# Performance work log

Measured on AMD Instinct MI355X. Metric: run time of the kernel, lower is better.

The kernel has to match this reference:

```python
import jax, jax.numpy as jnp
import numpy as np

N = 100000   # nodes / embedding vocab
E = 1600000  # edges
D = 128      # feature dim
R = 7        # num relations
B = 4096     # matches
EPS = 1e-5


def setup_inputs() -> dict:
    key = jax.random.key(0)
    ks = jax.random.split(key, 12)
    s = 0.05
    return {
        "x": jnp.arange(N, dtype=jnp.int32),
        "edge_index": jax.random.randint(ks[0], (2, E), 0, N, dtype=jnp.int32),
        "edge_type": jax.random.randint(ks[1], (E,), 0, R, dtype=jnp.int32),
        "home": jax.random.randint(ks[2], (B,), 0, N, dtype=jnp.int32),
        "away": jax.random.randint(ks[3], (B,), 0, N, dtype=jnp.int32),
        "embed": jax.random.normal(ks[4], (N, D), jnp.float32) * s,
        "rel_w": jax.random.normal(ks[5], (3, R, D, D), jnp.float32) * s,
        "root_w": jax.random.normal(ks[6], (3, D, D), jnp.float32) * s,
        "conv_b": jnp.zeros((3, D), jnp.float32),
        "bn_gamma": jnp.ones((2, D), jnp.float32),
        "bn_beta": jnp.zeros((2, D), jnp.float32),
        "bn_mean": jnp.zeros((2, D), jnp.float32),
        "bn_var": jnp.ones((2, D), jnp.float32),
        "fc0_w": jax.random.normal(ks[7], (256, 2 * D), jnp.float32) * s,
        "fc0_b": jnp.zeros((256,), jnp.float32),
        "fc1_w": jax.random.normal(ks[8], (128, 256), jnp.float32) * s,
        "fc1_b": jnp.zeros((128,), jnp.float32),
        "fc2_w": jax.random.normal(ks[9], (3, 128), jnp.float32) * s,
        "fc2_b": jnp.zeros((3,), jnp.float32),
    }


def rgcn_conv(h, rel_w, root_w, bias, src, dst, seg):
    # PyG RGCNConv with aggr='mean': per-relation mean of source features,
    # aggregate-then-transform (valid since the relation transform is linear).
    n = h.shape[0]
    agg = jax.ops.segment_sum(h[src], seg, num_segments=n * R)      # [N*R, Din]
    cnt = jax.ops.segment_sum(jnp.ones((src.shape[0],), h.dtype), seg,
                              num_segments=n * R)                   # [N*R]
    agg = (agg / jnp.maximum(cnt, 1.0)[:, None]).reshape(n, R, -1)  # [N, R, Din]
    return jnp.einsum('nri,rio->no', agg, rel_w) + h @ root_w + bias


def reference(x, edge_index, edge_type, home, away, embed, rel_w, root_w, conv_b,
              bn_gamma, bn_beta, bn_mean, bn_var,
              fc0_w, fc0_b, fc1_w, fc1_b, fc2_w, fc2_b):
    src, dst = edge_index[0], edge_index[1]
    seg = dst.astype(jnp.int32) * R + edge_type  # combined (node, relation) id

    h = embed[x]  # [N, D]
    for l in range(2):
        h = rgcn_conv(h, rel_w[l], root_w[l], conv_b[l], src, dst, seg)
        h = (h - bn_mean[l]) * jax.lax.rsqrt(bn_var[l] + EPS) * bn_gamma[l] + bn_beta[l]
        h = jax.nn.relu(h)
    h = rgcn_conv(h, rel_w[2], root_w[2], conv_b[2], src, dst, seg)

    g = jnp.concatenate([h[home], h[away]], axis=1)  # [B, 2D]
    g = jax.nn.relu(g @ fc0_w.T + fc0_b)
    g = jax.nn.relu(g @ fc1_w.T + fc1_b)
    g = g @ fc2_w.T + fc2_b
    return jax.nn.log_softmax(g, axis=1)
```

## Files before the change

kernel.cpp:

```cpp
#include <hip/hip_runtime.h>
#include <hip/hip_bf16.h>

#define RR 7
#define EPSBN 1e-5f

typedef __attribute__((ext_vector_type(8))) __bf16 bf16x8;
typedef __attribute__((ext_vector_type(4))) float f32x4;
typedef __attribute__((ext_vector_type(2))) float f32x2;

__device__ __forceinline__ float uhi2f(unsigned int u) {
    union { unsigned int i; float f; } c; c.i = u; return c.f;
}
__device__ __forceinline__ unsigned short f2b(float f) {
    union { float f; unsigned int i; } c; c.f = f;
    unsigned int x = c.i;
    return (unsigned short)((x + 0x7fffu + ((x >> 16) & 1u)) >> 16);
}

__global__ void hist_k(const int* __restrict__ dst, const int* __restrict__ et,
                       int* __restrict__ cnt, int* __restrict__ rank, int ne) {
    int e = blockIdx.x * 256 + threadIdx.x;
    if (e < ne) rank[e] = atomicAdd(&cnt[dst[e] * RR + et[e]], 1);
}
__global__ void scan1_k(const int* __restrict__ cnt, int* __restrict__ bsum, int n) {
    __shared__ int sh[256];
    int base = blockIdx.x << 10;
    int s = 0;
    for (int i = threadIdx.x; i < 1024; i += 256) { int idx = base + i; if (idx < n) s += cnt[idx]; }
    sh[threadIdx.x] = s; __syncthreads();
    for (int off = 128; off > 0; off >>= 1) {
        if (threadIdx.x < off) sh[threadIdx.x] += sh[threadIdx.x + off];
        __syncthreads();
    }
    if (threadIdx.x == 0) bsum[blockIdx.x] = sh[0];
}
__global__ void scan2_k(int* __restrict__ bsum, int nb) {
    __shared__ int sh[256];
    int t = threadIdx.x;
    int v[4]; int loc = 0;
#pragma unroll
    for (int i = 0; i < 4; ++i) { int idx = t * 4 + i; v[i] = (idx < nb) ? bsum[idx] : 0; loc += v[i]; }
    sh[t] = loc; __syncthreads();
    for (int off = 1; off < 256; off <<= 1) {
        int x = (t >= off) ? sh[t - off] : 0;
        __syncthreads();
        sh[t] += x;
        __syncthreads();
    }
    int ex = (t > 0) ? sh[t - 1] : 0;
#pragma unroll
    for (int i = 0; i < 4; ++i) { int idx = t * 4 + i; if (idx < nb) { int vv = v[i]; bsum[idx] = ex; ex += vv; } }
}
__global__ void scan3_k(const int* __restrict__ cnt, const int* __restrict__ boff,
                        int* __restrict__ ptr, int n, int total) {
    __shared__ int sh[256];
    int t = threadIdx.x;
    int base = (blockIdx.x << 10) + (t << 2);
    int v[4]; int loc = 0;
#pragma unroll
    for (int i = 0; i < 4; ++i) { int idx = base + i; v[i] = (idx < n) ? cnt[idx] : 0; loc += v[i]; }
    sh[t] = loc; __syncthreads();
    for (int off = 1; off < 256; off <<= 1) {
        int x = (t >= off) ? sh[t - off] : 0;
        __syncthreads();
        sh[t] += x;
        __syncthreads();
    }
    int ex = boff[blockIdx.x] + ((t > 0) ? sh[t - 1] : 0);
#pragma unroll
    for (int i = 0; i < 4; ++i) {
        int idx = base + i;
        if (idx < n) { ptr[idx] = ex; ex += v[i]; }
    }
    if (blockIdx.x == 0 && t == 0) ptr[n] = total;
}
__global__ void scatter_k(const int* __restrict__ src, const int* __restrict__ dst,
                          const int* __restrict__ et, const int* __restrict__ rank,
                          const int* __restrict__ ptr, int* __restrict__ ssorted, int ne) {
    int e = blockIdx.x * 256 + threadIdx.x;
    if (e < ne) {
        int seg = dst[e] * RR + et[e];
        ssorted[ptr[seg] + rank[e]] = src[e];
    }
    if (blockIdx.x == 0 && threadIdx.x < 16) ssorted[ne + threadIdx.x] = 0;
}

__global__ void mark_k(const int* __restrict__ home, const int* __restrict__ away,
                       const int* __restrict__ ptr, const int* __restrict__ ssorted,
                       int* __restrict__ mark, int* __restrict__ list,
                       int* __restrict__ count, int Bn) {
    int i = blockIdx.x * 256 + threadIdx.x;
    if (i >= 2 * Bn) return;
    int node = (i < Bn) ? home[i] : away[i - Bn];
    if (atomicExch(&mark[node], 1) == 0) { int p = atomicAdd(count, 1); list[p] = node; }
    int e0 = ptr[node * RR], e1 = ptr[node * RR + RR];
    for (int e = e0; e < e1; ++e) {
        int s = ssorted[e];
        if (atomicExch(&mark[s], 1) == 0) { int p = atomicAdd(count, 1); list[p] = s; }
    }
}

__global__ __launch_bounds__(256) void prep_all_k(
    const float* __restrict__ rel_w, const float* __restrict__ root_w,
    unsigned short* __restrict__ wall,
    const int* __restrict__ x, const float* __restrict__ embed,
    unsigned short* __restrict__ h, int n, int nhb,
    const float* __restrict__ fc0w, const float* __restrict__ fc1w,
    float* __restrict__ w0t, float* __restrict__ w1t,
    const float* __restrict__ conv_b,
    const float* __restrict__ bn_g, const float* __restrict__ bn_b,
    const float* __restrict__ bn_m, const float* __restrict__ bn_v,
    float* __restrict__ AB)
{
    __shared__ unsigned short T[128][130];
    int b = blockIdx.x;
    int t = threadIdx.x;
    if (b < 24) {
        int l = b >> 3, kb = b & 7;
        const float* src = (kb < RR) ? rel_w + ((size_t)(l * RR + kb) << 14)
                                     : root_w + ((size_t)l << 14);
        for (int c = t; c < 4096; c += 256) {
            float4 f = *(const float4*)(src + (c << 2));
            int i = c >> 5, o = (c & 31) << 2;
            T[i][o] = f2b(f.x); T[i][o+1] = f2b(f.y); T[i][o+2] = f2b(f.z); T[i][o+3] = f2b(f.w);
        }
        __syncthreads();
        unsigned short* dst = wall + ((size_t)b << 14);
        for (int c = t; c < 2048; c += 256) {
            int frag = c >> 6;
            int lane = c & 63;
            int ks = frag >> 3, nt = frag & 7;
            int o = (nt << 4) + (lane & 15);
            int ib = (ks << 5) + ((lane >> 4) << 3);
            uint4 o4;
            o4.x = (unsigned)T[ib+0][o] | ((unsigned)T[ib+1][o] << 16);
            o4.y = (unsigned)T[ib+2][o] | ((unsigned)T[ib+3][o] << 16);
            o4.z = (unsigned)T[ib+4][o] | ((unsigned)T[ib+5][o] << 16);
            o4.w = (unsigned)T[ib+6][o] | ((unsigned)T[ib+7][o] << 16);
            *(uint4*)(dst + (c << 3)) = o4;
        }
    } else if (b < 24 + nhb) {
        int i = (b - 24) * 256 + t;
        if (i < n * 16) {
            int node = i >> 4, c8 = (i & 15) << 3;
            const float* e = embed + ((size_t)x[node] << 7) + c8;
            float4 f0 = *(const float4*)e;
            float4 f1 = *(const float4*)(e + 4);
            uint4 o4;
            o4.x = (unsigned)f2b(f0.x) | ((unsigned)f2b(f0.y) << 16);
            o4.y = (unsigned)f2b(f0.z) | ((unsigned)f2b(f0.w) << 16);
            o4.z = (unsigned)f2b(f1.x) | ((unsigned)f2b(f1.y) << 16);
            o4.w = (unsigned)f2b(f1.z) | ((unsigned)f2b(f1.w) << 16);
            *(uint4*)(h + ((size_t)node << 7) + c8) = o4;
        }
    } else if (b < 24 + nhb + 256) {
        int idx = ((b - 24 - nhb) << 8) + t;
        int o = idx & 255, i = idx >> 8;
        w0t[idx] = fc0w[o * 256 + i];
    } else if (b < 24 + nhb + 384) {
        int idx = ((b - 24 - nhb - 256) << 8) + t;
        int o = idx & 127, i = idx >> 7;
        w1t[idx] = fc1w[o * 256 + i];
    } else {
        for (int q = t; q < 384; q += 256) {
            int l = q >> 7, j = q & 127;
            float A = 1.f, Bv = conv_b[(l << 7) + j];
            if (l < 2) {
                float sc = bn_g[(l << 7) + j] * rsqrtf(bn_v[(l << 7) + j] + EPSBN);
                A = sc;
                Bv = Bv * sc + (bn_b[(l << 7) + j] - bn_m[(l << 7) + j] * sc);
            }
            AB[(l << 8) + j] = A;
            AB[(l << 8) + 128 + j] = Bv;
        }
    }
}

#define PAIRF(pw) ((f32x2){uhi2f((pw) << 16), uhi2f((pw) & 0xffff0000u)})
#define ACCP(b, u) { av2[(b)+0] += PAIRF((u).x); av2[(b)+1] += PAIRF((u).y); \
                     av2[(b)+2] += PAIRF((u).z); av2[(b)+3] += PAIRF((u).w); }
#define GATH(s) { const unsigned short* hp = h_in + ((size_t)(s) << 7) + (quad << 3); \
                  uint4 u0 = *(const uint4*)(hp);       uint4 u1 = *(const uint4*)(hp + 32); \
                  uint4 u2 = *(const uint4*)(hp + 64);  uint4 u3 = *(const uint4*)(hp + 96); \
                  ACCP(0, u0); ACCP(4, u1); ACCP(8, u2); ACCP(12, u3); }

__global__ __launch_bounds__(128, 4) void layer_k(
    const unsigned short* __restrict__ h_in,
    unsigned short* __restrict__ h_out,
    const unsigned short* __restrict__ wfrag,
    const float* __restrict__ AB,
    const int* __restrict__ seg_ptr, const int* __restrict__ src_sorted,
    const int* __restrict__ list_a, const int* __restrict__ list_b, int listB,
    const int* __restrict__ nout_dev,
    int nout, int bnrelu, int by_node)
{
    const int tid  = threadIdx.x;
    const int wave = tid >> 6;
    const int lane = tid & 63;
    const int n16  = lane & 15;
    const int quad = lane >> 4;
    const int row0 = blockIdx.x << 5;
    if (nout_dev) nout = *nout_dev;
    if (row0 >= nout) return;
    const int gidx = row0 + (wave << 4) + n16;
    const bool valid = gidx < nout;
    int gnode = 0;
    if (valid) {
        gnode = list_a ? (gidx < listB ? list_a[gidx] : list_b[gidx - listB]) : gidx;
    }

    int p[8];
    {
        int b = valid ? gnode * RR : 0;
#pragma unroll
        for (int i = 0; i < 8; ++i) p[i] = seg_ptr[b + i];
    }

    f32x4 acc[8];
#pragma unroll
    for (int i = 0; i < 8; ++i) acc[i] = (f32x4){0.f, 0.f, 0.f, 0.f};

    int sv0, sv1, sv2, sv3;
    { int e0 = p[0]; sv0 = src_sorted[e0]; sv1 = src_sorted[e0+1];
      sv2 = src_sorted[e0+2]; sv3 = src_sorted[e0+3]; }

    const unsigned short* wl = wfrag + (lane << 3);

#pragma unroll
    for (int kb = 0; kb < 8; ++kb) {
        f32x2 av2[16];
#pragma unroll
        for (int i = 0; i < 16; ++i) av2[i] = (f32x2){0.f, 0.f};
        float scale = 1.f;
        int nv0 = 0, nv1 = 0, nv2 = 0, nv3 = 0;
        if (kb < RR) {
            if (kb < RR - 1) {
                int en = p[kb + 1];
                nv0 = src_sorted[en]; nv1 = src_sorted[en+1];
                nv2 = src_sorted[en+2]; nv3 = src_sorted[en+3];
            }
            if (valid) {
                int e0 = p[kb], e1 = p[kb + 1];
                int cnt = e1 - e0;
                if (cnt > 0) scale = __builtin_amdgcn_rcpf((float)cnt);
                if (cnt > 0) GATH(sv0);
                if (cnt > 1) GATH(sv1);
                if (cnt > 2) GATH(sv2);
                if (cnt > 3) GATH(sv3);
                for (int e = e0 + 4; e < e1; ++e) {
                    int s = src_sorted[e];
                    GATH(s);
                }
            }
        } else {
            if (valid) GATH(gnode);
        }
        uint4 au[4];
#pragma unroll
        for (int ks = 0; ks < 4; ++ks) {
            unsigned pw[4];
#pragma unroll
            for (int m = 0; m < 4; ++m) {
                f32x2 q = av2[(ks << 2) + m] * scale;
                __hip_bfloat162 b2 = __float22bfloat162_rn(make_float2(q.x, q.y));
                unsigned uu; __builtin_memcpy(&uu, &b2, 4);
                pw[m] = uu;
            }
            au[ks].x = pw[0]; au[ks].y = pw[1]; au[ks].z = pw[2]; au[ks].w = pw[3];
        }
        const unsigned short* wk = wl + (kb << 14);
#pragma unroll
        for (int ks = 0; ks < 4; ++ks) {
            bf16x8 af;
            __builtin_memcpy(&af, &au[ks], 16);
#pragma unroll
            for (int nt = 0; nt < 8; ++nt) {
                bf16x8 bfr = *(const bf16x8*)(wk + (((ks << 3) + nt) << 9));
                acc[nt] = __builtin_amdgcn_mfma_f32_16x16x32_bf16(af, bfr, acc[nt], 0, 0, 0);
            }
        }
        sv0 = nv0; sv1 = nv1; sv2 = nv2; sv3 = nv3;
    }

    int orow[4];
#pragma unroll
    for (int r = 0; r < 4; ++r) {
        int ri = row0 + (wave << 4) + (quad << 2) + r;
        if (ri < nout) {
            orow[r] = by_node ? (ri < listB ? list_a[ri] : list_b[ri - listB]) : ri;
        } else orow[r] = -1;
    }
#pragma unroll
    for (int nt = 0; nt < 8; ++nt) {
        int j = (nt << 4) + n16;
        float Aj = AB[j];
        float Bj = AB[128 + j];
#pragma unroll
        for (int r = 0; r < 4; ++r) {
            if (orow[r] >= 0) {
                float v = acc[nt][r] * Aj + Bj;
                if (bnrelu) v = fmaxf(v, 0.f);
                h_out[((size_t)orow[r] << 7) + j] = f2b(v);
            }
        }
    }
}

__global__ __launch_bounds__(256) void mlp_k(
    const unsigned short* __restrict__ hC,
    const float* __restrict__ w0t, const float* __restrict__ bb0,
    const float* __restrict__ w1t, const float* __restrict__ bb1,
    const float* __restrict__ w2, const float* __restrict__ bb2,
    float* __restrict__ out, int Bn)
{
    __shared__ __attribute__((aligned(16))) float g0[16][256];
    __shared__ __attribute__((aligned(16))) float g1[16][256];
    __shared__ float lg[16][4];
    int t = threadIdx.x;
    {
        int row = t >> 4;
        int cseg = (t & 15) << 4;
        int gr = (blockIdx.x << 4) + row;
        int gc = (gr < Bn) ? gr : 0;
        const unsigned short* sp = (cseg < 128) ? (hC + ((size_t)gc << 7) + cseg)
                                                : (hC + ((size_t)(Bn + gc) << 7) + (cseg - 128));
#pragma unroll
        for (int c8 = 0; c8 < 2; ++c8) {
            uint4 v = *(const uint4*)(sp + (c8 << 3));
            int base = cseg + (c8 << 3);
            g0[row][base+0] = uhi2f(v.x << 16); g0[row][base+1] = uhi2f(v.x & 0xffff0000u);
            g0[row][base+2] = uhi2f(v.y << 16); g0[row][base+3] = uhi2f(v.y & 0xffff0000u);
            g0[row][base+4] = uhi2f(v.z << 16); g0[row][base+5] = uhi2f(v.z & 0xffff0000u);
            g0[row][base+6] = uhi2f(v.w << 16); g0[row][base+7] = uhi2f(v.w & 0xffff0000u);
        }
    }
    __syncthreads();
    {
        float acc[16];
#pragma unroll
        for (int r = 0; r < 16; ++r) acc[r] = 0.f;
#pragma unroll 4
        for (int i = 0; i < 256; ++i) {
            float w = w0t[(i << 8) + t];
#pragma unroll
            for (int r = 0; r < 16; ++r) acc[r] += w * g0[r][i];
        }
        float bb = bb0[t];
#pragma unroll
        for (int r = 0; r < 16; ++r) g1[r][t] = fmaxf(acc[r] + bb, 0.f);
    }
    __syncthreads();
    {
        int o = t & 127, rg = t >> 7;
        float acc[8];
#pragma unroll
        for (int r = 0; r < 8; ++r) acc[r] = 0.f;
#pragma unroll 4
        for (int i = 0; i < 256; ++i) {
            float w = w1t[(i << 7) + o];
#pragma unroll
            for (int r = 0; r < 8; ++r) acc[r] += w * g1[(rg << 3) + r][i];
        }
        float bb = bb1[o];
#pragma unroll
        for (int r = 0; r < 8; ++r) g0[(rg << 3) + r][o] = fmaxf(acc[r] + bb, 0.f);
    }
    __syncthreads();
    if (t < 48) {
        int row = t / 3, cls = t - row * 3;
        const float* wr = w2 + (cls << 7);
        float a = 0.f;
        for (int i = 0; i < 128; i += 4) {
            float4 w = *(const float4*)(wr + i);
            float4 g = *(const float4*)&g0[row][i];
            a += w.x * g.x + w.y * g.y + w.z * g.z + w.w * g.w;
        }
        lg[row][cls] = a + bb2[cls];
    }
    __syncthreads();
    if (t < 16) {
        int gr = (blockIdx.x << 4) + t;
        if (gr < Bn) {
            float l0 = lg[t][0], l1 = lg[t][1], l2 = lg[t][2];
            float m = fmaxf(l0, fmaxf(l1, l2));
            float lse = m + logf(expf(l0 - m) + expf(l1 - m) + expf(l2 - m));
            out[gr * 3 + 0] = l0 - lse;
            out[gr * 3 + 1] = l1 - lse;
            out[gr * 3 + 2] = l2 - lse;
        }
    }
}

extern "C" void kernel_launch(void* const* d_in, const int* in_sizes, int n_in,
                              void* d_out, int out_size, void* d_ws, size_t ws_size,
                              hipStream_t stream) {
    const int*   x      = (const int*)d_in[0];
    const int*   eidx   = (const int*)d_in[1];
    const int*   etype  = (const int*)d_in[2];
    const int*   home   = (const int*)d_in[3];
    const int*   away   = (const int*)d_in[4];
    const float* embed  = (const float*)d_in[5];
    const float* rel_w  = (const float*)d_in[6];
    const float* root_w = (const float*)d_in[7];
    const float* conv_b = (const float*)d_in[8];
    const float* bn_g   = (const float*)d_in[9];
    const float* bn_b   = (const float*)d_in[10];
    const float* bn_m   = (const float*)d_in[11];
    const float* bn_v   = (const float*)d_in[12];
    const float* fc0w   = (const float*)d_in[13];
    const float* fc0b   = (const float*)d_in[14];
    const float* fc1w   = (const float*)d_in[15];
    const float* fc1b   = (const float*)d_in[16];
    const float* fc2w   = (const float*)d_in[17];
    const float* fc2b   = (const float*)d_in[18];
    float* out = (float*)d_out;

    const int N_ = in_sizes[0];
    const int E_ = in_sizes[2];
    const int B_ = in_sizes[3];
    const int NS = N_ * RR;

    char* ws = (char*)d_ws;
    auto alloc = [&](size_t bytes) -> char* {
        char* p = ws;
        ws += (bytes + 255) & ~(size_t)255;
        return p;
    };
    int* zreg        = (int*)alloc((size_t)(NS + N_ + 1) * 4);
    int* cursor      = zreg;
    int* mark        = zreg + NS;
    int* fcount      = zreg + NS + N_;
    int* ptr         = (int*)alloc((size_t)(NS + 1) * 4);
    int* bsum        = (int*)alloc(4096);
    int* rank        = (int*)alloc((size_t)E_ * 4);
    int* src_sorted  = (int*)alloc((size_t)(E_ + 16) * 4);
    int* flist       = (int*)alloc((size_t)N_ * 4);
    unsigned short* wall = (unsigned short*)alloc((size_t)3 * 8 * 16384 * 2);
    unsigned short* hA   = (unsigned short*)alloc((size_t)N_ * 128 * 2);
    unsigned short* hB   = (unsigned short*)alloc((size_t)N_ * 128 * 2);
    unsigned short* hC   = (unsigned short*)alloc((size_t)2 * B_ * 128 * 2);
    float* AB        = (float*)alloc(3 * 256 * 4);
    float* w0t       = (float*)alloc(65536 * 4);
    float* w1t       = (float*)alloc(32768 * 4);

    const int nb = (NS + 1023) / 1024;
    const int nhb = (N_ * 16 + 255) / 256;

    (void)hipMemsetAsync(zreg, 0, (size_t)(NS + N_ + 1) * 4, stream);
    hist_k<<<(E_ + 255) / 256, 256, 0, stream>>>(eidx + E_, etype, cursor, rank, E_);
    scan1_k<<<nb, 256, 0, stream>>>(cursor, bsum, NS);
    scan2_k<<<1, 256, 0, stream>>>(bsum, nb);
    scan3_k<<<nb, 256, 0, stream>>>(cursor, bsum, ptr, NS, E_);
    scatter_k<<<(E_ + 255) / 256, 256, 0, stream>>>(eidx, eidx + E_, etype, rank, ptr,
                                                    src_sorted, E_);

    mark_k<<<(2 * B_ + 255) / 256, 256, 0, stream>>>(home, away, ptr, src_sorted,
                                                     mark, flist, fcount, B_);

    prep_all_k<<<24 + nhb + 384 + 1, 256, 0, stream>>>(
        rel_w, root_w, wall, x, embed, hA, N_, nhb,
        fc0w, fc1w, w0t, w1t, conv_b, bn_g, bn_b, bn_m, bn_v, AB);

    const int lgrid = (N_ + 31) / 32;
    layer_k<<<lgrid, 128, 0, stream>>>(hA, hB, wall + 0 * 8 * 16384, AB + 0,
                                       ptr, src_sorted, nullptr, nullptr, 0,
                                       nullptr, N_, 1, 0);
    layer_k<<<lgrid, 128, 0, stream>>>(hB, hA, wall + 1 * 8 * 16384, AB + 256,
                                       ptr, src_sorted, flist, flist, N_,
                                       fcount, N_, 1, 1);
    const int n3 = 2 * B_;
    layer_k<<<(n3 + 31) / 32, 128, 0, stream>>>(hA, hC, wall + 2 * 8 * 16384, AB + 512,
                                                ptr, src_sorted, home, away, B_,
                                                nullptr, n3, 0, 0);

    mlp_k<<<(B_ + 15) / 16, 256, 0, stream>>>(hC, w0t, fc0b, w1t, fc1b,
                                              fc2w, fc2b, out, B_);
}
```

Measured before the change: 647.1 us.

## Fold frontier marking into hist/scatter, drop scan2, halve MLP rows per block

Home/away marking moves into the histogram kernel, and the frontier list is built inside the scatter kernel by checking the destination's mark. This removes the separate mark_k launch and its serial per-node edge loops. The single-block scan2 kernel is replaced by each scan3 block summing the preceding block sums itself, which saves a launch at the cost of redundant reads. The MLP kernel now handles 8 rows per block instead of 16, doubling its grid for more parallelism but loading the weights more times.

```diff
diff --git a/kernel.cpp b/kernel.cpp
--- a/kernel.cpp
+++ b/kernel.cpp
@@ -18,9 +18,19 @@
 }
 
 __global__ void hist_k(const int* __restrict__ dst, const int* __restrict__ et,
-                       int* __restrict__ cnt, int* __restrict__ rank, int ne) {
-    int e = blockIdx.x * 256 + threadIdx.x;
-    if (e < ne) rank[e] = atomicAdd(&cnt[dst[e] * RR + et[e]], 1);
+                       int* __restrict__ cnt, int* __restrict__ rank, int ne, int hbase,
+                       const int* __restrict__ home, const int* __restrict__ away,
+                       int* __restrict__ mark, int Bn) {
+    int gid = blockIdx.x * 256 + threadIdx.x;
+    if (gid < ne) {
+        rank[gid] = atomicAdd(&cnt[dst[gid] * RR + et[gid]], 1);
+    } else {
+        int hi = gid - hbase;
+        if (hi >= 0 && hi < 2 * Bn) {
+            int node = (hi < Bn) ? home[hi] : away[hi - Bn];
+            atomicOr(&mark[node], 1);
+        }
+    }
 }
 __global__ void scan1_k(const int* __restrict__ cnt, int* __restrict__ bsum, int n) {
     __shared__ int sh[256];
@@ -34,27 +44,22 @@
     }
     if (threadIdx.x == 0) bsum[blockIdx.x] = sh[0];
 }
-__global__ void scan2_k(int* __restrict__ bsum, int nb) {
-    __shared__ int sh[256];
-    int t = threadIdx.x;
-    int v[4]; int loc = 0;
-#pragma unroll
-    for (int i = 0; i < 4; ++i) { int idx = t * 4 + i; v[i] = (idx < nb) ? bsum[idx] : 0; loc += v[i]; }
-    sh[t] = loc; __syncthreads();
-    for (int off = 1; off < 256; off <<= 1) {
-        int x = (t >= off) ? sh[t - off] : 0;
-        __syncthreads();
-        sh[t] += x;
-        __syncthreads();
-    }
-    int ex = (t > 0) ? sh[t - 1] : 0;
-#pragma unroll
-    for (int i = 0; i < 4; ++i) { int idx = t * 4 + i; if (idx < nb) { int vv = v[i]; bsum[idx] = ex; ex += vv; } }
-}
-__global__ void scan3_k(const int* __restrict__ cnt, const int* __restrict__ boff,
+__global__ void scan3_k(const int* __restrict__ cnt, const int* __restrict__ bsum,
                         int* __restrict__ ptr, int n, int total) {
     __shared__ int sh[256];
+    __shared__ int boffs;
     int t = threadIdx.x;
+    {
+        int s = 0;
+        for (int i = t; i < blockIdx.x; i += 256) s += bsum[i];
+        sh[t] = s; __syncthreads();
+        for (int off = 128; off > 0; off >>= 1) {
+            if (t < off) sh[t] += sh[t + off];
+            __syncthreads();
+        }
+        if (t == 0) boffs = sh[0];
+        __syncthreads();
+    }
     int base = (blockIdx.x << 10) + (t << 2);
     int v[4]; int loc = 0;
 #pragma unroll
@@ -66,7 +71,7 @@
         sh[t] += x;
         __syncthreads();
     }
-    int ex = boff[blockIdx.x] + ((t > 0) ? sh[t - 1] : 0);
+    int ex = boffs + ((t > 0) ? sh[t - 1] : 0);
 #pragma unroll
     for (int i = 0; i < 4; ++i) {
         int idx = base + i;
@@ -76,28 +81,27 @@
 }
 __global__ void scatter_k(const int* __restrict__ src, const int* __restrict__ dst,
                           const int* __restrict__ et, const int* __restrict__ rank,
-                          const int* __restrict__ ptr, int* __restrict__ ssorted, int ne) {
-    int e = blockIdx.x * 256 + threadIdx.x;
-    if (e < ne) {
-        int seg = dst[e] * RR + et[e];
-        ssorted[ptr[seg] + rank[e]] = src[e];
+                          const int* __restrict__ ptr, int* __restrict__ ssorted,
+                          int ne, int hbase,
+                          const int* __restrict__ home, const int* __restrict__ away,
+                          int* __restrict__ mark, int* __restrict__ flist,
+                          int* __restrict__ fcount, int Bn) {
+    int gid = blockIdx.x * 256 + threadIdx.x;
+    if (gid < ne) {
+        int d = dst[gid], s = src[gid];
+        int seg = d * RR + et[gid];
+        ssorted[ptr[seg] + rank[gid]] = s;
+        if (mark[d] & 1) {
+            if (!(atomicOr(&mark[s], 2) & 2)) { int p = atomicAdd(fcount, 1); flist[p] = s; }
+        }
+    } else {
+        int hi = gid - hbase;
+        if (hi >= 0 && hi < 2 * Bn) {
+            int node = (hi < Bn) ? home[hi] : away[hi - Bn];
+            if (!(atomicOr(&mark[node], 2) & 2)) { int p = atomicAdd(fcount, 1); flist[p] = node; }
+        }
     }
     if (blockIdx.x == 0 && threadIdx.x < 16) ssorted[ne + threadIdx.x] = 0;
-}
-
-__global__ void mark_k(const int* __restrict__ home, const int* __restrict__ away,
-                       const int* __restrict__ ptr, const int* __restrict__ ssorted,
-                       int* __restrict__ mark, int* __restrict__ list,
-                       int* __restrict__ count, int Bn) {
-    int i = blockIdx.x * 256 + threadIdx.x;
-    if (i >= 2 * Bn) return;
-    int node = (i < Bn) ? home[i] : away[i - Bn];
-    if (atomicExch(&mark[node], 1) == 0) { int p = atomicAdd(count, 1); list[p] = node; }
-    int e0 = ptr[node * RR], e1 = ptr[node * RR + RR];
-    for (int e = e0; e < e1; ++e) {
-        int s = ssorted[e];
-        if (atomicExch(&mark[s], 1) == 0) { int p = atomicAdd(count, 1); list[p] = s; }
-    }
 }
 
 __global__ __launch_bounds__(256) void prep_all_k(
@@ -313,60 +317,56 @@
     const float* __restrict__ w2, const float* __restrict__ bb2,
     float* __restrict__ out, int Bn)
 {
-    __shared__ __attribute__((aligned(16))) float g0[16][256];
-    __shared__ __attribute__((aligned(16))) float g1[16][256];
-    __shared__ float lg[16][4];
+    __shared__ __attribute__((aligned(16))) float g0[8][256];
+    __shared__ __attribute__((aligned(16))) float g1[8][256];
+    __shared__ float lg[8][4];
     int t = threadIdx.x;
     {
-        int row = t >> 4;
-        int cseg = (t & 15) << 4;
-        int gr = (blockIdx.x << 4) + row;
+        int row = t >> 5;
+        int cseg = (t & 31) << 3;
+        int gr = (blockIdx.x << 3) + row;
         int gc = (gr < Bn) ? gr : 0;
         const unsigned short* sp = (cseg < 128) ? (hC + ((size_t)gc << 7) + cseg)
                                                 : (hC + ((size_t)(Bn + gc) << 7) + (cseg - 128));
-#pragma unroll
-        for (int c8 = 0; c8 < 2; ++c8) {
-            uint4 v = *(const uint4*)(sp + (c8 << 3));
-            int base = cseg + (c8 << 3);
-            g0[row][base+0] = uhi2f(v.x << 16); g0[row][base+1] = uhi2f(v.x & 0xffff0000u);
-            g0[row][base+2] = uhi2f(v.y << 16); g0[row][base+3] = uhi2f(v.y & 0xffff0000u);
-            g0[row][base+4] = uhi2f(v.z << 16); g0[row][base+5] = uhi2f(v.z & 0xffff0000u);
-            g0[row][base+6] = uhi2f(v.w << 16); g0[row][base+7] = uhi2f(v.w & 0xffff0000u);
-        }
+        uint4 v = *(const uint4*)sp;
+        g0[row][cseg+0] = uhi2f(v.x << 16); g0[row][cseg+1] = uhi2f(v.x & 0xffff0000u);
+        g0[row][cseg+2] = uhi2f(v.y << 16); g0[row][cseg+3] = uhi2f(v.y & 0xffff0000u);
+        g0[row][cseg+4] = uhi2f(v.z << 16); g0[row][cseg+5] = uhi2f(v.z & 0xffff0000u);
+        g0[row][cseg+6] = uhi2f(v.w << 16); g0[row][cseg+7] = uhi2f(v.w & 0xffff0000u);
     }
     __syncthreads();
     {
-        float acc[16];
-#pragma unroll
-        for (int r = 0; r < 16; ++r) acc[r] = 0.f;
+        float acc[8];
+#pragma unroll
+        for (int r = 0; r < 8; ++r) acc[r] = 0.f;
 #pragma unroll 4
         for (int i = 0; i < 256; ++i) {
             float w = w0t[(i << 8) + t];
 #pragma unroll
-            for (int r = 0; r < 16; ++r) acc[r] += w * g0[r][i];
+            for (int r = 0; r < 8; ++r) acc[r] += w * g0[r][i];
         }
         float bb = bb0[t];
 #pragma unroll
-        for (int r = 0; r < 16; ++r) g1[r][t] = fmaxf(acc[r] + bb, 0.f);
+        for (int r = 0; r < 8; ++r) g1[r][t] = fmaxf(acc[r] + bb, 0.f);
     }
     __syncthreads();
     {
         int o = t & 127, rg = t >> 7;
-        float acc[8];
-#pragma unroll
-        for (int r = 0; r < 8; ++r) acc[r] = 0.f;
+        float acc[4];
+#pragma unroll
+        for (int r = 0; r < 4; ++r) acc[r] = 0.f;
 #pragma unroll 4
         for (int i = 0; i < 256; ++i) {
             float w = w1t[(i << 7) + o];
 #pragma unroll
-            for (int r = 0; r < 8; ++r) acc[r] += w * g1[(rg << 3) + r][i];
+            for (int r = 0; r < 4; ++r) acc[r] += w * g1[(rg << 2) + r][i];
         }
         float bb = bb1[o];
 #pragma unroll
-        for (int r = 0; r < 8; ++r) g0[(rg << 3) + r][o] = fmaxf(acc[r] + bb, 0.f);
+        for (int r = 0; r < 4; ++r) g0[(rg << 2) + r][o] = fmaxf(acc[r] + bb, 0.f);
     }
     __syncthreads();
-    if (t < 48) {
+    if (t < 24) {
         int row = t / 3, cls = t - row * 3;
         const float* wr = w2 + (cls << 7);
         float a = 0.f;
@@ -378,8 +378,8 @@
         lg[row][cls] = a + bb2[cls];
     }
     __syncthreads();
-    if (t < 16) {
-        int gr = (blockIdx.x << 4) + t;
+    if (t < 8) {
+        int gr = (blockIdx.x << 3) + t;
         if (gr < Bn) {
             float l0 = lg[t][0], l1 = lg[t][1], l2 = lg[t][2];
             float m = fmaxf(l0, fmaxf(l1, l2));
@@ -443,19 +443,20 @@
     float* w0t       = (float*)alloc(65536 * 4);
     float* w1t       = (float*)alloc(32768 * 4);
 
-    const int nb = (NS + 1023) / 1024;
+    const int nb  = (NS + 1023) / 1024;
     const int nhb = (N_ * 16 + 255) / 256;
+    const int ebk = (E_ + 255) / 256;
+    const int hbase = ebk * 256;
+    const int hbk = (2 * B_ + 255) / 256;
 
     (void)hipMemsetAsync(zreg, 0, (size_t)(NS + N_ + 1) * 4, stream);
-    hist_k<<<(E_ + 255) / 256, 256, 0, stream>>>(eidx + E_, etype, cursor, rank, E_);
+    hist_k<<<ebk + hbk, 256, 0, stream>>>(eidx + E_, etype, cursor, rank, E_, hbase,
+                                          home, away, mark, B_);
     scan1_k<<<nb, 256, 0, stream>>>(cursor, bsum, NS);
-    scan2_k<<<1, 256, 0, stream>>>(bsum, nb);
     scan3_k<<<nb, 256, 0, stream>>>(cursor, bsum, ptr, NS, E_);
-    scatter_k<<<(E_ + 255) / 256, 256, 0, stream>>>(eidx, eidx + E_, etype, rank, ptr,
-                                                    src_sorted, E_);
-
-    mark_k<<<(2 * B_ + 255) / 256, 256, 0, stream>>>(home, away, ptr, src_sorted,
-                                                     mark, flist, fcount, B_);
+    scatter_k<<<ebk + hbk, 256, 0, stream>>>(eidx, eidx + E_, etype, rank, ptr,
+                                             src_sorted, E_, hbase,
+                                             home, away, mark, flist, fcount, B_);
 
     prep_all_k<<<24 + nhb + 384 + 1, 256, 0, stream>>>(
         rel_w, root_w, wall, x, embed, hA, N_, nhb,
@@ -473,6 +474,6 @@
                                                 ptr, src_sorted, home, away, B_,
                                                 nullptr, n3, 0, 0);
 
-    mlp_k<<<(B_ + 15) / 16, 256, 0, stream>>>(hC, w0t, fc0b, w1t, fc1b,
-                                              fc2w, fc2b, out, B_);
-}
+    mlp_k<<<(B_ + 7) / 8, 256, 0, stream>>>(hC, w0t, fc0b, w1t, fc1b,
+                                            fc2w, fc2b, out, B_);
+}
```

Measured after the change: 821.0 us. +26.9%, slower.
